# Kernel tuning notes

Hardware: AMD Instinct MI355X
Metric: run time of the kernel (lower is better)

The kernel has to match this reference:

```python
import jax, jax.numpy as jnp
import numpy as np

B, S, D, H = 2, 2048, 1024, 16
DK = D // H  # 64
SQRT_DK = DK ** 0.5
NEG = -1e9


def setup_inputs() -> dict:
    key = jax.random.key(0)
    ks = jax.random.split(key, 7)
    scale = 1.0 / np.sqrt(D)
    return {
        "x": jax.random.normal(ks[0], (B, S, D), jnp.float32),
        "encoder_output": jax.random.normal(ks[1], (B, S, D), jnp.float32),
        "mask": jax.random.randint(ks[2], (B, S), 0, 2, jnp.int32),
        "WQ": jax.random.normal(ks[3], (D, D), jnp.float32) * scale,
        "WK": jax.random.normal(ks[4], (D, D), jnp.float32) * scale,
        "WV": jax.random.normal(ks[5], (D, D), jnp.float32) * scale,
        "WO": jax.random.normal(ks[6], (D, D), jnp.float32) * scale,
    }


def reference(x, encoder_output, mask, WQ, WK, WV, WO):
    b, s, d = x.shape
    # project and split heads: (b, h, s, dk)
    q = (x @ WQ).reshape(b, s, H, DK).transpose(0, 2, 1, 3)
    k = (encoder_output @ WK).reshape(b, s, H, DK).transpose(0, 2, 1, 3)
    v = (encoder_output @ WV).reshape(b, s, H, DK).transpose(0, 2, 1, 3)
    # scores: (b, h, s_q, s_k)
    scores = jnp.einsum('bhqd,bhkd->bhqk', q, k) / SQRT_DK
    # future mask (strict upper triangle) + padding mask broadcast over key dim
    future = jnp.triu(jnp.ones((s, s), jnp.int32), 1)  # (s, s)
    m = mask[:, None, :, None] + future[None, None, :, :]  # (b, 1->h, s_q, s_k)
    scores = jnp.where(m != 0, NEG, scores)
    attn = jax.nn.softmax(scores, axis=-1)
    # context: (b, s, h, dk) -> (b, s, d)
    ctx = jnp.einsum('bhqk,bhkd->bqhd', attn, v).reshape(b, s, d)
    return ctx @ WO
```

## Files before the change

kernel.cpp:

```cpp
#include <hip/hip_runtime.h>
#include <hip/hip_bf16.h>

constexpr int B = 2, S = 2048, D = 1024, H = 16, DK = 64;
constexpr int M = B * S;
constexpr float LOG2E = 1.44269504088896f;
constexpr float NEGBIG = -3.0e38f;
constexpr float QSCALE = 0.125f * LOG2E;

using short8 = __attribute__((ext_vector_type(8))) short;
using short4v = __attribute__((ext_vector_type(4))) short;
using f32x4 = __attribute__((ext_vector_type(4))) float;

#define GLOBAL_AS __attribute__((address_space(1)))
#define LDS_AS __attribute__((address_space(3)))

__device__ __forceinline__ void gll16(const void* g, void* l) {
  __builtin_amdgcn_global_load_lds((const GLOBAL_AS void*)g, (LDS_AS void*)l, 16, 0, 0);
}

__device__ __forceinline__ short f2bf(float f) {
  __hip_bfloat16 h = __float2bfloat16(f);
  short s;
  __builtin_memcpy(&s, &h, 2);
  return s;
}
__device__ __forceinline__ float bf2f(short s) {
  __hip_bfloat16 h;
  __builtin_memcpy(&h, &s, 2);
  return __bfloat162float(h);
}
__device__ __forceinline__ unsigned pack2bf(float a, float b) {
  return (unsigned)(unsigned short)f2bf(a) | ((unsigned)(unsigned short)f2bf(b) << 16);
}

__global__ __launch_bounds__(256) void cvt_bf16_kernel(const float* __restrict__ x,
                                                       const float* __restrict__ enc,
                                                       short* __restrict__ xb,
                                                       short* __restrict__ encb) {
  const int i = blockIdx.x * 256 + threadIdx.x;
  const float4 v = ((const float4*)(blockIdx.y ? enc : x))[i];
  short4v o;
  o[0] = f2bf(v.x); o[1] = f2bf(v.y); o[2] = f2bf(v.z); o[3] = f2bf(v.w);
  ((short4v*)(blockIdx.y ? encb : xb))[i] = o;
}

__global__ __launch_bounds__(256) void transw_kernel(const float* __restrict__ W0,
                                                     const float* __restrict__ W1,
                                                     const float* __restrict__ W2,
                                                     const float* __restrict__ W3,
                                                     short* __restrict__ Wt) {
  __shared__ float t[64][65];
  const int z = blockIdx.z;
  const float* W = z == 0 ? W0 : z == 1 ? W1 : z == 2 ? W2 : W3;
  short* dst = Wt + (size_t)z * D * D;
  const int k0 = blockIdx.y * 64, n0 = blockIdx.x * 64;
  const int lx = threadIdx.x & 63, ly = threadIdx.x >> 6;
  #pragma unroll
  for (int r = 0; r < 64; r += 4)
    t[r + ly][lx] = W[(size_t)(k0 + r + ly) * D + n0 + lx];
  __syncthreads();
  #pragma unroll
  for (int r = 0; r < 64; r += 4)
    dst[(size_t)(n0 + r + ly) * D + k0 + lx] = f2bf(t[lx][r + ly]);
}

template <int QKV>
__global__ __launch_bounds__(256) void gemm_kernel(const short* __restrict__ A0,
                                                   const short* __restrict__ A1,
                                                   const short* __restrict__ Wts,
                                                   void* __restrict__ Cv) {
  __shared__ short As[2][4][128][8];
  __shared__ short Bs[2][4][128][8];
  const int z = QKV ? blockIdx.z : 0;
  const short* __restrict__ A = (QKV && z) ? A1 : A0;
  const short* __restrict__ Bt = Wts + (size_t)z * D * D;
  const float oscale = (QKV && z == 0) ? QSCALE : 1.0f;

  const int tid = threadIdx.x;
  const int lane = tid & 63, wid = tid >> 6;
  const int l15 = lane & 15, lg = lane >> 4;
  const int row0 = blockIdx.y * 128, col0 = blockIdx.x * 128;
  const int wm = wid >> 1, wn = wid & 1;
  f32x4 acc[4][4] = {};

  auto stage = [&](int k0, int nb) {
    #pragma unroll
    for (int it = 0; it < 2; ++it) {
      const int t = tid + it * 256;
      const int row = t & 127, kc2 = t >> 7;
      gll16(&A[(size_t)(row0 + row) * D + k0 + kc2 * 8],
            (char*)As + nb * 8192 + (wid * 64 + it * 256) * 16);
      gll16(&Bt[(size_t)(col0 + row) * D + k0 + kc2 * 8],
            (char*)Bs + nb * 8192 + (wid * 64 + it * 256) * 16);
    }
  };

  stage(0, 0);
  __syncthreads();
  int cur = 0;
  for (int t = 0; t < D / 32; ++t) {
    if (t < D / 32 - 1) stage((t + 1) * 32, cur ^ 1);
    short8 af[4], bfr[4];
    #pragma unroll
    for (int m = 0; m < 4; ++m) af[m] = *(const short8*)&As[cur][lg][wm * 64 + m * 16 + l15][0];
    #pragma unroll
    for (int n = 0; n < 4; ++n) bfr[n] = *(const short8*)&Bs[cur][lg][wn * 64 + n * 16 + l15][0];
    #pragma unroll
    for (int m = 0; m < 4; ++m)
      #pragma unroll
      for (int n = 0; n < 4; ++n)
        acc[m][n] = __builtin_amdgcn_mfma_f32_16x16x32_bf16(af[m], bfr[n], acc[m][n], 0, 0, 0);
    __syncthreads();
    cur ^= 1;
  }
  #pragma unroll
  for (int m = 0; m < 4; ++m) {
    #pragma unroll
    for (int r = 0; r < 4; ++r) {
      const int row = row0 + wm * 64 + m * 16 + 4 * lg + r;
      #pragma unroll
      for (int n = 0; n < 4; ++n) {
        const int col = col0 + wn * 64 + n * 16 + l15;
        if (QKV)
          ((short*)Cv)[(size_t)z * M * D + (size_t)row * D + col] = f2bf(acc[m][n][r] * oscale);
        else
          ((float*)Cv)[(size_t)row * D + col] = acc[m][n][r];
      }
    }
  }
}

__global__ __launch_bounds__(256) void vmean_part_kernel(const short* __restrict__ Vb,
                                                         float* __restrict__ part) {
  const int d = blockIdx.x * 256 + threadIdx.x;
  const int c = blockIdx.y;
  const int b = blockIdx.z;
  float s = 0.f;
  for (int i = 0; i < S / 16; ++i)
    s += bf2f(Vb[(size_t)(b * S + c * (S / 16) + i) * D + d]);
  part[((size_t)b * 16 + c) * D + d] = s;
}
__global__ __launch_bounds__(256) void vmean_final_kernel(const float* __restrict__ part,
                                                          float* __restrict__ vmean) {
  const int d = blockIdx.x * 256 + threadIdx.x;
  const int b = blockIdx.y;
  float s = 0.f;
  #pragma unroll
  for (int c = 0; c < 16; ++c) s += part[((size_t)b * 16 + c) * D + d];
  vmean[(size_t)b * D + d] = s * (1.0f / S);
}

__device__ __forceinline__ int keyof(int c, int i) {
  return ((c >> 1) << 5) + ((i >> 2) << 3) + ((c & 1) << 2) + (i & 3);
}
__device__ __forceinline__ int vt_byte(int kc, int d, int ksb) {
  return kc * 1024 + ((d ^ (kc & 7)) << 4) + ksb * 2;
}

__global__ __launch_bounds__(256) void attn_kernel(const short* __restrict__ Qb,
                                                   const short* __restrict__ Kb,
                                                   const short* __restrict__ Vb,
                                                   const int* __restrict__ maskp,
                                                   const float* __restrict__ vmean,
                                                   short* __restrict__ ctxb) {
  __shared__ short KsBuf[2][4096];
  __shared__ short VtBuf[2][4096];
  const int h = blockIdx.x, iblk = blockIdx.y, b = blockIdx.z;
  const int qtA = iblk, qtB = 31 - iblk;
  const int tid = threadIdx.x, lane = tid & 63, wid = tid >> 6;
  const int l15 = lane & 15, lg = lane >> 4;

  short8 qfA[2], qfB[2];
  {
    const size_t oA = (size_t)(b * S + qtA * 64 + wid * 16 + l15) * D + h * DK;
    const size_t oB = (size_t)(b * S + qtB * 64 + wid * 16 + l15) * D + h * DK;
    qfA[0] = *(const short8*)&Qb[oA + lg * 8];
    qfA[1] = *(const short8*)&Qb[oA + 32 + lg * 8];
    qfB[0] = *(const short8*)&Qb[oB + lg * 8];
    qfB[1] = *(const short8*)&Qb[oB + 32 + lg * 8];
  }
  float mA = NEGBIG, lA = 0.f, mB = NEGBIG, lB = 0.f;
  f32x4 cA[4] = {}, cB[4] = {};

  const int kkey = keyof(lane >> 4, lane & 15);
  const int vu = tid & 31, ve = tid >> 5;

  auto stageK = [&](int j, int nb) {
    const size_t rowbase = (size_t)(b * S + j * 64 + kkey) * D + h * DK;
    #pragma unroll
    for (int it = 0; it < 2; ++it) {
      const int dc = wid * 2 + it;
      gll16(&Kb[rowbase + dc * 8], (char*)KsBuf + nb * 8192 + dc * 1024);
    }
  };
  auto loadV = [&](int j, short8& va, short8& vb2) {
    const size_t vb0 = (size_t)(b * S + j * 64 + 2 * vu) * D + h * DK + ve * 8;
    va = *(const short8*)&Vb[vb0];
    vb2 = *(const short8*)&Vb[vb0 + D];
  };
  auto writeV = [&](int nb, const short8& va, const short8& vb2) {
    const int kc = vu >> 2, ksb = (vu & 3) * 2;
    #pragma unroll
    for (int i = 0; i < 8; ++i) {
      const unsigned w = (unsigned)(unsigned short)va[i] | ((unsigned)(unsigned short)vb2[i] << 16);
      *(unsigned*)((char*)VtBuf + nb * 8192 + vt_byte(kc, ve * 8 + i, ksb)) = w;
    }
  };

  auto tile = [&](const short8* qf, float& m, float& l, f32x4* cx, bool diag, int nb) {
    const char* ksb_ = (const char*)KsBuf + nb * 8192;
    const char* vtb_ = (const char*)VtBuf + nb * 8192;
    f32x4 sa[4];
    __builtin_amdgcn_s_setprio(1);
    #pragma unroll
    for (int c = 0; c < 4; ++c) {
      const short8 kf0 = *(const short8*)(ksb_ + lg * 1024 + c * 256 + l15 * 16);
      const short8 kf1 = *(const short8*)(ksb_ + (4 + lg) * 1024 + c * 256 + l15 * 16);
      f32x4 zz = {0.f, 0.f, 0.f, 0.f};
      zz = __builtin_amdgcn_mfma_f32_16x16x32_bf16(kf0, qf[0], zz, 0, 0, 0);
      zz = __builtin_amdgcn_mfma_f32_16x16x32_bf16(kf1, qf[1], zz, 0, 0, 0);
      sa[c] = zz;
    }
    __builtin_amdgcn_s_setprio(0);
    if (diag) {
      const int ql = wid * 16 + l15;
      #pragma unroll
      for (int c = 0; c < 4; ++c)
        #pragma unroll
        for (int r = 0; r < 4; ++r)
          if (((c >> 1) << 5) + (lg << 3) + ((c & 1) << 2) + r > ql) sa[c][r] = NEGBIG;
    }
    float pm = sa[0][0];
    #pragma unroll
    for (int c = 0; c < 4; ++c)
      #pragma unroll
      for (int r = 0; r < 4; ++r) pm = fmaxf(pm, sa[c][r]);
    pm = fmaxf(pm, __shfl_xor(pm, 16));
    pm = fmaxf(pm, __shfl_xor(pm, 32));
    if (pm > m + 8.f) {
      const float sc = exp2f(m - pm);
      l *= sc;
      #pragma unroll
      for (int dt = 0; dt < 4; ++dt) cx[dt] *= sc;
      m = pm;
    }
    float rs = 0.f;
    #pragma unroll
    for (int c = 0; c < 4; ++c)
      #pragma unroll
      for (int r = 0; r < 4; ++r) {
        const float p = exp2f(sa[c][r] - m);
        sa[c][r] = p;
        rs += p;
      }
    rs += __shfl_xor(rs, 16);
    rs += __shfl_xor(rs, 32);
    l += rs;
    short8 pf[2];
    #pragma unroll
    for (int kk = 0; kk < 2; ++kk)
      #pragma unroll
      for (int jj = 0; jj < 8; ++jj)
        pf[kk][jj] = f2bf(sa[kk * 2 + (jj >> 2)][jj & 3]);
    __builtin_amdgcn_s_setprio(1);
    #pragma unroll
    for (int kk = 0; kk < 2; ++kk)
      #pragma unroll
      for (int dt = 0; dt < 4; ++dt) {
        const short8 vf = *(const short8*)(vtb_ + vt_byte(kk * 4 + lg, dt * 16 + l15, 0));
        cx[dt] = __builtin_amdgcn_mfma_f32_16x16x32_bf16(vf, pf[kk], cx[dt], 0, 0, 0);
      }
    __builtin_amdgcn_s_setprio(0);
  };

  {
    short8 va, vb2;
    stageK(0, 0);
    loadV(0, va, vb2);
    writeV(0, va, vb2);
  }
  __syncthreads();
  int cur = 0;
  for (int j = 0; j <= qtB; ++j) {
    short8 nva, nvb;
    if (j < qtB) { stageK(j + 1, cur ^ 1); loadV(j + 1, nva, nvb); }
    tile(qfB, mB, lB, cB, j == qtB, cur);
    if (j <= qtA) tile(qfA, mA, lA, cA, j == qtA, cur);
    if (j < qtB) writeV(cur ^ 1, nva, nvb);
    __syncthreads();
    cur ^= 1;
  }

  auto epi = [&](float l, const f32x4* cx, int qt) {
    const int qg = qt * 64 + wid * 16 + l15;
    const int mq = maskp[b * S + qg];
    const float inv = 1.0f / l;
    short* orow = &ctxb[(size_t)(b * S + qg) * D + h * DK];
    const float* vmb = &vmean[(size_t)b * D + h * DK];
    #pragma unroll
    for (int dt = 0; dt < 4; ++dt)
      #pragma unroll
      for (int p2 = 0; p2 < 2; ++p2) {
        const int d = dt * 16 + 4 * lg + p2 * 2;
        const float v0 = mq ? vmb[d]     : cx[dt][p2 * 2] * inv;
        const float v1 = mq ? vmb[d + 1] : cx[dt][p2 * 2 + 1] * inv;
        *(unsigned*)&orow[d] = pack2bf(v0, v1);
      }
  };
  epi(lA, cA, qtA);
  epi(lB, cB, qtB);
}

extern "C" void kernel_launch(void* const* d_in, const int* in_sizes, int n_in,
                              void* d_out, int out_size, void* d_ws, size_t ws_size,
                              hipStream_t stream) {
  (void)in_sizes; (void)n_in; (void)out_size; (void)ws_size;
  const float* x   = (const float*)d_in[0];
  const float* enc = (const float*)d_in[1];
  const int*   msk = (const int*)d_in[2];
  const float* WQ  = (const float*)d_in[3];
  const float* WK  = (const float*)d_in[4];
  const float* WV  = (const float*)d_in[5];
  const float* WO  = (const float*)d_in[6];
  float* out = (float*)d_out;

  char* ws = (char*)d_ws;
  const size_t MB = 1u << 20;
  short* xb    = (short*)(ws + 0);
  short* encb  = (short*)(ws + 8 * MB);
  short* Qb    = (short*)(ws + 16 * MB);
  short* WQt   = (short*)(ws + 40 * MB);
  float* vpart = (float*)(ws + 48 * MB);
  float* vmean = (float*)(ws + 48 * MB + 131072);
  short* Kb    = Qb + (size_t)M * D;
  short* Vb    = Kb + (size_t)M * D;
  short* WOt   = WQt + (size_t)3 * D * D;
  short* ctxb  = xb;

  cvt_bf16_kernel<<<dim3(M * D / 4 / 256, 2), 256, 0, stream>>>(x, enc, xb, encb);
  transw_kernel<<<dim3(16, 16, 4), 256, 0, stream>>>(WQ, WK, WV, WO, WQt);

  gemm_kernel<1><<<dim3(D / 128, M / 128, 3), 256, 0, stream>>>(xb, encb, WQt, Qb);

  vmean_part_kernel<<<dim3(D / 256, 16, B), 256, 0, stream>>>(Vb, vpart);
  vmean_final_kernel<<<dim3(D / 256, B), 256, 0, stream>>>(vpart, vmean);

  attn_kernel<<<dim3(H, 16, B), 256, 0, stream>>>(Qb, Kb, Vb, msk, vmean, ctxb);

  gemm_kernel<0><<<dim3(D / 128, M / 128, 1), 256, 0, stream>>>(ctxb, nullptr, WOt, out);
}
```

Baseline: 189.3 us.

## Fuse prep kernels, fold V-mean into QKV GEMM, split attention waves

Merges the bf16 conversion and weight transpose into one launch, and computes the V column sums inside the QKV GEMM epilogue with atomics instead of two separate reduction kernels. The attention kernel moves to 512 threads, so the two query tiles of each block run on separate wave groups instead of serially in the same waves. The output GEMM uses 128x64 tiles to launch more blocks. The aim is fewer launches and better parallelism, at the cost of a memset, atomic contention, and idle waves in the group handling the shorter causal tile.

```diff
diff --git a/kernel.cpp b/kernel.cpp
--- a/kernel.cpp
+++ b/kernel.cpp
@@ -33,48 +33,53 @@
   return (unsigned)(unsigned short)f2bf(a) | ((unsigned)(unsigned short)f2bf(b) << 16);
 }
 
-__global__ __launch_bounds__(256) void cvt_bf16_kernel(const float* __restrict__ x,
-                                                       const float* __restrict__ enc,
-                                                       short* __restrict__ xb,
-                                                       short* __restrict__ encb) {
-  const int i = blockIdx.x * 256 + threadIdx.x;
-  const float4 v = ((const float4*)(blockIdx.y ? enc : x))[i];
-  short4v o;
-  o[0] = f2bf(v.x); o[1] = f2bf(v.y); o[2] = f2bf(v.z); o[3] = f2bf(v.w);
-  ((short4v*)(blockIdx.y ? encb : xb))[i] = o;
-}
-
-__global__ __launch_bounds__(256) void transw_kernel(const float* __restrict__ W0,
-                                                     const float* __restrict__ W1,
-                                                     const float* __restrict__ W2,
-                                                     const float* __restrict__ W3,
-                                                     short* __restrict__ Wt) {
+__global__ __launch_bounds__(256) void prep_kernel(const float* __restrict__ x,
+                                                   const float* __restrict__ enc,
+                                                   const float* __restrict__ W0,
+                                                   const float* __restrict__ W1,
+                                                   const float* __restrict__ W2,
+                                                   const float* __restrict__ W3,
+                                                   short* __restrict__ xb,
+                                                   short* __restrict__ encb,
+                                                   short* __restrict__ Wt) {
   __shared__ float t[64][65];
-  const int z = blockIdx.z;
-  const float* W = z == 0 ? W0 : z == 1 ? W1 : z == 2 ? W2 : W3;
-  short* dst = Wt + (size_t)z * D * D;
-  const int k0 = blockIdx.y * 64, n0 = blockIdx.x * 64;
-  const int lx = threadIdx.x & 63, ly = threadIdx.x >> 6;
-  #pragma unroll
-  for (int r = 0; r < 64; r += 4)
-    t[r + ly][lx] = W[(size_t)(k0 + r + ly) * D + n0 + lx];
-  __syncthreads();
-  #pragma unroll
-  for (int r = 0; r < 64; r += 4)
-    dst[(size_t)(n0 + r + ly) * D + k0 + lx] = f2bf(t[lx][r + ly]);
-}
-
-template <int QKV>
-__global__ __launch_bounds__(256) void gemm_kernel(const short* __restrict__ A0,
-                                                   const short* __restrict__ A1,
-                                                   const short* __restrict__ Wts,
-                                                   void* __restrict__ Cv) {
+  const int bx = blockIdx.x;
+  if (bx < 8192) {
+    const float4* src = (const float4*)((bx & 4096) ? enc : x);
+    short4v* dst = (short4v*)((bx & 4096) ? encb : xb);
+    const int i = (bx & 4095) * 256 + threadIdx.x;
+    const float4 v = src[i];
+    short4v o;
+    o[0] = f2bf(v.x); o[1] = f2bf(v.y); o[2] = f2bf(v.z); o[3] = f2bf(v.w);
+    dst[i] = o;
+  } else {
+    const int idx = bx - 8192;
+    const int z = idx >> 8, rem = idx & 255;
+    const float* W = z == 0 ? W0 : z == 1 ? W1 : z == 2 ? W2 : W3;
+    short* dstw = Wt + (size_t)z * D * D;
+    const int n0 = (rem & 15) * 64, k0 = (rem >> 4) * 64;
+    const int lx = threadIdx.x & 63, ly = threadIdx.x >> 6;
+    #pragma unroll
+    for (int r = 0; r < 64; r += 4)
+      t[r + ly][lx] = W[(size_t)(k0 + r + ly) * D + n0 + lx];
+    __syncthreads();
+    #pragma unroll
+    for (int r = 0; r < 64; r += 4)
+      dstw[(size_t)(n0 + r + ly) * D + k0 + lx] = f2bf(t[lx][r + ly]);
+  }
+}
+
+__global__ __launch_bounds__(256) void gemm_qkv_kernel(const short* __restrict__ A0,
+                                                       const short* __restrict__ A1,
+                                                       const short* __restrict__ Wts,
+                                                       short* __restrict__ Cv,
+                                                       float* __restrict__ vsum) {
   __shared__ short As[2][4][128][8];
   __shared__ short Bs[2][4][128][8];
-  const int z = QKV ? blockIdx.z : 0;
-  const short* __restrict__ A = (QKV && z) ? A1 : A0;
+  const int z = blockIdx.z;
+  const short* __restrict__ A = z ? A1 : A0;
   const short* __restrict__ Bt = Wts + (size_t)z * D * D;
-  const float oscale = (QKV && z == 0) ? QSCALE : 1.0f;
+  const float oscale = (z == 0) ? QSCALE : 1.0f;
 
   const int tid = threadIdx.x;
   const int lane = tid & 63, wid = tid >> 6;
@@ -86,8 +91,8 @@
   auto stage = [&](int k0, int nb) {
     #pragma unroll
     for (int it = 0; it < 2; ++it) {
-      const int t = tid + it * 256;
-      const int row = t & 127, kc2 = t >> 7;
+      const int c = tid + it * 256;
+      const int row = c & 127, kc2 = c >> 7;
       gll16(&A[(size_t)(row0 + row) * D + k0 + kc2 * 8],
             (char*)As + nb * 8192 + (wid * 64 + it * 256) * 16);
       gll16(&Bt[(size_t)(col0 + row) * D + k0 + kc2 * 8],
@@ -121,33 +126,76 @@
       #pragma unroll
       for (int n = 0; n < 4; ++n) {
         const int col = col0 + wn * 64 + n * 16 + l15;
-        if (QKV)
-          ((short*)Cv)[(size_t)z * M * D + (size_t)row * D + col] = f2bf(acc[m][n][r] * oscale);
-        else
-          ((float*)Cv)[(size_t)row * D + col] = acc[m][n][r];
+        Cv[(size_t)z * M * D + (size_t)row * D + col] = f2bf(acc[m][n][r] * oscale);
       }
     }
   }
-}
-
-__global__ __launch_bounds__(256) void vmean_part_kernel(const short* __restrict__ Vb,
-                                                         float* __restrict__ part) {
-  const int d = blockIdx.x * 256 + threadIdx.x;
-  const int c = blockIdx.y;
-  const int b = blockIdx.z;
-  float s = 0.f;
-  for (int i = 0; i < S / 16; ++i)
-    s += bf2f(Vb[(size_t)(b * S + c * (S / 16) + i) * D + d]);
-  part[((size_t)b * 16 + c) * D + d] = s;
-}
-__global__ __launch_bounds__(256) void vmean_final_kernel(const float* __restrict__ part,
-                                                          float* __restrict__ vmean) {
-  const int d = blockIdx.x * 256 + threadIdx.x;
-  const int b = blockIdx.y;
-  float s = 0.f;
+  if (z == 2) {
+    const int bidx = row0 >> 11;
+    #pragma unroll
+    for (int n = 0; n < 4; ++n) {
+      float s = 0.f;
+      #pragma unroll
+      for (int m = 0; m < 4; ++m)
+        s += acc[m][n][0] + acc[m][n][1] + acc[m][n][2] + acc[m][n][3];
+      s += __shfl_xor(s, 16);
+      s += __shfl_xor(s, 32);
+      if (lg == 0) atomicAdd(&vsum[(size_t)bidx * D + col0 + wn * 64 + n * 16 + l15], s);
+    }
+  }
+}
+
+__global__ __launch_bounds__(256) void gemmO_kernel(const short* __restrict__ A,
+                                                    const short* __restrict__ Bt,
+                                                    float* __restrict__ C) {
+  __shared__ short As[2][4][128][8];
+  __shared__ short Bs[2][4][64][8];
+  const int tid = threadIdx.x;
+  const int lane = tid & 63, wid = tid >> 6;
+  const int l15 = lane & 15, lg = lane >> 4;
+  const int col0 = blockIdx.x * 64, row0 = blockIdx.y * 128;
+  const int wm = wid >> 1, wn = wid & 1;
+  f32x4 acc[4][2] = {};
+
+  auto stage = [&](int k0, int nb) {
+    #pragma unroll
+    for (int it = 0; it < 2; ++it) {
+      const int c = tid + it * 256;
+      const int row = c & 127, kc2 = c >> 7;
+      gll16(&A[(size_t)(row0 + row) * D + k0 + kc2 * 8],
+            (char*)As + nb * 8192 + (wid * 64 + it * 256) * 16);
+    }
+    gll16(&Bt[(size_t)(col0 + lane) * D + k0 + wid * 8],
+          (char*)Bs + nb * 4096 + wid * 1024);
+  };
+
+  stage(0, 0);
+  __syncthreads();
+  int cur = 0;
+  for (int t = 0; t < D / 32; ++t) {
+    if (t < D / 32 - 1) stage((t + 1) * 32, cur ^ 1);
+    short8 af[4], bfr[2];
+    #pragma unroll
+    for (int m = 0; m < 4; ++m) af[m] = *(const short8*)&As[cur][lg][wm * 64 + m * 16 + l15][0];
+    #pragma unroll
+    for (int n = 0; n < 2; ++n) bfr[n] = *(const short8*)&Bs[cur][lg][wn * 32 + n * 16 + l15][0];
+    #pragma unroll
+    for (int m = 0; m < 4; ++m)
+      #pragma unroll
+      for (int n = 0; n < 2; ++n)
+        acc[m][n] = __builtin_amdgcn_mfma_f32_16x16x32_bf16(af[m], bfr[n], acc[m][n], 0, 0, 0);
+    __syncthreads();
+    cur ^= 1;
+  }
   #pragma unroll
-  for (int c = 0; c < 16; ++c) s += part[((size_t)b * 16 + c) * D + d];
-  vmean[(size_t)b * D + d] = s * (1.0f / S);
+  for (int m = 0; m < 4; ++m)
+    #pragma unroll
+    for (int r = 0; r < 4; ++r) {
+      const int row = row0 + wm * 64 + m * 16 + 4 * lg + r;
+      #pragma unroll
+      for (int n = 0; n < 2; ++n)
+        C[(size_t)row * D + col0 + wn * 32 + n * 16 + l15] = acc[m][n][r];
+    }
 }
 
 __device__ __forceinline__ int keyof(int c, int i) {
@@ -157,57 +205,52 @@
   return kc * 1024 + ((d ^ (kc & 7)) << 4) + ksb * 2;
 }
 
-__global__ __launch_bounds__(256) void attn_kernel(const short* __restrict__ Qb,
-                                                   const short* __restrict__ Kb,
-                                                   const short* __restrict__ Vb,
-                                                   const int* __restrict__ maskp,
-                                                   const float* __restrict__ vmean,
-                                                   short* __restrict__ ctxb) {
+__global__ __launch_bounds__(512, 4) void attn_kernel(const short* __restrict__ Qb,
+                                                      const short* __restrict__ Kb,
+                                                      const short* __restrict__ Vb,
+                                                      const int* __restrict__ maskp,
+                                                      const float* __restrict__ vsum,
+                                                      short* __restrict__ ctxb) {
   __shared__ short KsBuf[2][4096];
   __shared__ short VtBuf[2][4096];
   const int h = blockIdx.x, iblk = blockIdx.y, b = blockIdx.z;
   const int qtA = iblk, qtB = 31 - iblk;
   const int tid = threadIdx.x, lane = tid & 63, wid = tid >> 6;
+  const int grp = wid >> 2, wq = wid & 3;
+  const int qt = grp ? qtB : qtA;
   const int l15 = lane & 15, lg = lane >> 4;
 
-  short8 qfA[2], qfB[2];
+  short8 qf[2];
   {
-    const size_t oA = (size_t)(b * S + qtA * 64 + wid * 16 + l15) * D + h * DK;
-    const size_t oB = (size_t)(b * S + qtB * 64 + wid * 16 + l15) * D + h * DK;
-    qfA[0] = *(const short8*)&Qb[oA + lg * 8];
-    qfA[1] = *(const short8*)&Qb[oA + 32 + lg * 8];
-    qfB[0] = *(const short8*)&Qb[oB + lg * 8];
-    qfB[1] = *(const short8*)&Qb[oB + 32 + lg * 8];
-  }
-  float mA = NEGBIG, lA = 0.f, mB = NEGBIG, lB = 0.f;
-  f32x4 cA[4] = {}, cB[4] = {};
-
-  const int kkey = keyof(lane >> 4, lane & 15);
-  const int vu = tid & 31, ve = tid >> 5;
+    const size_t o = (size_t)(b * S + qt * 64 + wq * 16 + l15) * D + h * DK;
+    qf[0] = *(const short8*)&Qb[o + lg * 8];
+    qf[1] = *(const short8*)&Qb[o + 32 + lg * 8];
+  }
+  float m = NEGBIG, l = 0.f;
+  f32x4 cx[4] = {};
+
+  const int kkey = keyof(lg, l15);
+  const int vu = tid & 31, dv = tid >> 5;
+  const int vkc = vu >> 2, vksb = (vu & 3) * 2;
 
   auto stageK = [&](int j, int nb) {
-    const size_t rowbase = (size_t)(b * S + j * 64 + kkey) * D + h * DK;
-    #pragma unroll
-    for (int it = 0; it < 2; ++it) {
-      const int dc = wid * 2 + it;
-      gll16(&Kb[rowbase + dc * 8], (char*)KsBuf + nb * 8192 + dc * 1024);
-    }
-  };
-  auto loadV = [&](int j, short8& va, short8& vb2) {
-    const size_t vb0 = (size_t)(b * S + j * 64 + 2 * vu) * D + h * DK + ve * 8;
-    va = *(const short8*)&Vb[vb0];
-    vb2 = *(const short8*)&Vb[vb0 + D];
-  };
-  auto writeV = [&](int nb, const short8& va, const short8& vb2) {
-    const int kc = vu >> 2, ksb = (vu & 3) * 2;
-    #pragma unroll
-    for (int i = 0; i < 8; ++i) {
+    gll16(&Kb[(size_t)(b * S + j * 64 + kkey) * D + h * DK + wid * 8],
+          (char*)KsBuf + nb * 8192 + wid * 1024);
+  };
+  auto loadV = [&](int j, short4v& va, short4v& vb2) {
+    const size_t vb0 = (size_t)(b * S + j * 64 + 2 * vu) * D + h * DK + dv * 4;
+    va = *(const short4v*)&Vb[vb0];
+    vb2 = *(const short4v*)&Vb[vb0 + D];
+  };
+  auto writeV = [&](int nb, const short4v& va, const short4v& vb2) {
+    #pragma unroll
+    for (int i = 0; i < 4; ++i) {
       const unsigned w = (unsigned)(unsigned short)va[i] | ((unsigned)(unsigned short)vb2[i] << 16);
-      *(unsigned*)((char*)VtBuf + nb * 8192 + vt_byte(kc, ve * 8 + i, ksb)) = w;
-    }
-  };
-
-  auto tile = [&](const short8* qf, float& m, float& l, f32x4* cx, bool diag, int nb) {
+      *(unsigned*)((char*)VtBuf + nb * 8192 + vt_byte(vkc, dv * 4 + i, vksb)) = w;
+    }
+  };
+
+  auto tile = [&](bool diag, int nb) {
     const char* ksb_ = (const char*)KsBuf + nb * 8192;
     const char* vtb_ = (const char*)VtBuf + nb * 8192;
     f32x4 sa[4];
@@ -223,7 +266,7 @@
     }
     __builtin_amdgcn_s_setprio(0);
     if (diag) {
-      const int ql = wid * 16 + l15;
+      const int ql = wq * 16 + l15;
       #pragma unroll
       for (int c = 0; c < 4; ++c)
         #pragma unroll
@@ -274,7 +317,7 @@
   };
 
   {
-    short8 va, vb2;
+    short4v va, vb2;
     stageK(0, 0);
     loadV(0, va, vb2);
     writeV(0, va, vb2);
@@ -282,33 +325,31 @@
   __syncthreads();
   int cur = 0;
   for (int j = 0; j <= qtB; ++j) {
-    short8 nva, nvb;
+    short4v nva, nvb;
     if (j < qtB) { stageK(j + 1, cur ^ 1); loadV(j + 1, nva, nvb); }
-    tile(qfB, mB, lB, cB, j == qtB, cur);
-    if (j <= qtA) tile(qfA, mA, lA, cA, j == qtA, cur);
+    if (j <= qt) tile(j == qt, cur);
     if (j < qtB) writeV(cur ^ 1, nva, nvb);
     __syncthreads();
     cur ^= 1;
   }
 
-  auto epi = [&](float l, const f32x4* cx, int qt) {
-    const int qg = qt * 64 + wid * 16 + l15;
+  {
+    const int qg = qt * 64 + wq * 16 + l15;
     const int mq = maskp[b * S + qg];
     const float inv = 1.0f / l;
+    constexpr float vscale = 1.0f / S;
     short* orow = &ctxb[(size_t)(b * S + qg) * D + h * DK];
-    const float* vmb = &vmean[(size_t)b * D + h * DK];
+    const float* vmb = &vsum[(size_t)b * D + h * DK];
     #pragma unroll
     for (int dt = 0; dt < 4; ++dt)
       #pragma unroll
       for (int p2 = 0; p2 < 2; ++p2) {
         const int d = dt * 16 + 4 * lg + p2 * 2;
-        const float v0 = mq ? vmb[d]     : cx[dt][p2 * 2] * inv;
-        const float v1 = mq ? vmb[d + 1] : cx[dt][p2 * 2 + 1] * inv;
+        const float v0 = mq ? vmb[d] * vscale     : cx[dt][p2 * 2] * inv;
+        const float v1 = mq ? vmb[d + 1] * vscale : cx[dt][p2 * 2 + 1] * inv;
         *(unsigned*)&orow[d] = pack2bf(v0, v1);
       }
-  };
-  epi(lA, cA, qtA);
-  epi(lB, cB, qtB);
+  }
 }
 
 extern "C" void kernel_launch(void* const* d_in, const int* in_sizes, int n_in,
@@ -330,22 +371,19 @@
   short* encb  = (short*)(ws + 8 * MB);
   short* Qb    = (short*)(ws + 16 * MB);
   short* WQt   = (short*)(ws + 40 * MB);
-  float* vpart = (float*)(ws + 48 * MB);
-  float* vmean = (float*)(ws + 48 * MB + 131072);
+  float* vsum  = (float*)(ws + 48 * MB);
   short* Kb    = Qb + (size_t)M * D;
   short* Vb    = Kb + (size_t)M * D;
   short* WOt   = WQt + (size_t)3 * D * D;
   short* ctxb  = xb;
 
-  cvt_bf16_kernel<<<dim3(M * D / 4 / 256, 2), 256, 0, stream>>>(x, enc, xb, encb);
-  transw_kernel<<<dim3(16, 16, 4), 256, 0, stream>>>(WQ, WK, WV, WO, WQt);
-
-  gemm_kernel<1><<<dim3(D / 128, M / 128, 3), 256, 0, stream>>>(xb, encb, WQt, Qb);
-
-  vmean_part_kernel<<<dim3(D / 256, 16, B), 256, 0, stream>>>(Vb, vpart);
-  vmean_final_kernel<<<dim3(D / 256, B), 256, 0, stream>>>(vpart, vmean);
-
-  attn_kernel<<<dim3(H, 16, B), 256, 0, stream>>>(Qb, Kb, Vb, msk, vmean, ctxb);
-
-  gemm_kernel<0><<<dim3(D / 128, M / 128, 1), 256, 0, stream>>>(ctxb, nullptr, WOt, out);
-}
+  hipMemsetAsync(vsum, 0, (size_t)B * D * sizeof(float), stream);
+
+  prep_kernel<<<dim3(9216), 256, 0, stream>>>(x, enc, WQ, WK, WV, WO, xb, encb, WQt);
+
+  gemm_qkv_kernel<<<dim3(D / 128, M / 128, 3), 256, 0, stream>>>(xb, encb, WQt, Qb, vsum);
+
+  attn_kernel<<<dim3(H, 16, B), 512, 0, stream>>>(Qb, Kb, Vb, msk, vsum, ctxb);
+
+  gemmO_kernel<<<dim3(D / 64, M / 128), 256, 0, stream>>>(ctxb, WOt, out);
+}
```

After: 183.0 us. 1.03x faster.
